# Performance work log

Hardware: AMD Instinct MI355X
Metric: run time of the kernel (lower is better)

## Reference

```python
import jax, jax.numpy as jnp
import numpy as np

B, C, H, W = 4, 64, 256, 256
P = 8            # patch size for rfft2 correlation
THETA = 10000.0  # RoPE base
EPS = 1e-6       # RMSNorm eps


def setup_inputs() -> dict:
    key = jax.random.key(0)
    ks = jax.random.split(key, 4)
    s = 0.05
    return {
        "x": jax.random.normal(ks[0], (B, C, H, W), jnp.float32),
        "w_hidden": jax.random.normal(ks[1], (6 * C, C), jnp.float32) * s,   # 1x1 conv dim->6dim
        "w_dw": jax.random.normal(ks[2], (6 * C, 1, 3, 3), jnp.float32) * s,  # depthwise 3x3
        "w_proj": jax.random.normal(ks[3], (C, 2 * C), jnp.float32) * s,      # 1x1 conv 2dim->dim
        "g_norm": jnp.ones((2 * C,), jnp.float32),
        "g_qnorm": jnp.ones((2 * C,), jnp.float32),
        "g_knorm": jnp.ones((2 * C,), jnp.float32),
    }


def _rms2d(x, w):
    # RMSNorm over channel dim of (B,C,H,W), computed in fp32, learned scale w[C]
    xf = x.astype(jnp.float32)
    var = jnp.mean(xf * xf, axis=1, keepdims=True)
    return w[None, :, None, None] * (xf * jax.lax.rsqrt(var + EPS))


def _rope2d(x):
    # 2D RoPE on (B, 2d, H, W): first d channels get row freqs, last d get col freqs.
    b, c2, h, w = x.shape
    d = c2 // 2
    n = d // 2
    inv = 1.0 / (THETA ** (jnp.arange(0, d, 2, dtype=jnp.float32)[:n] / d))  # (d//2,)
    fh = jnp.repeat(jnp.arange(h, dtype=jnp.float32)[:, None] * inv, 2, axis=-1)  # (h, d)
    fw = jnp.repeat(jnp.arange(w, dtype=jnp.float32)[:, None] * inv, 2, axis=-1)  # (w, d)
    freqs = jnp.concatenate(
        [jnp.broadcast_to(fh[:, None, :], (h, w, d)),
         jnp.broadcast_to(fw[None, :, :], (h, w, d))], axis=-1)  # (h, w, 2d)
    cos = jnp.moveaxis(jnp.cos(freqs), -1, 0)[None]  # (1, 2d, h, w)
    sin = jnp.moveaxis(jnp.sin(freqs), -1, 0)[None]
    xr = x.reshape(b, c2 // 2, 2, h, w)
    rot = jnp.stack([-xr[:, :, 1], xr[:, :, 0]], axis=2).reshape(b, c2, h, w)  # rotate_half
    return x * cos + rot * sin


def reference(x, w_hidden, w_dw, w_proj, g_norm, g_qnorm, g_knorm):
    # FSAS_V5 forward: 1x1 expand -> DW conv -> split q,k,v -> QK RMSNorm -> 2D RoPE
    # -> per-8x8-patch rfft2 correlation -> RMSNorm -> v * corr -> 1x1 project
    hidden = jnp.einsum('oi,bihw->bohw', w_hidden, x)
    hidden = jax.lax.conv_general_dilated(
        hidden, w_dw, window_strides=(1, 1), padding=((1, 1), (1, 1)),
        feature_group_count=w_dw.shape[0],
        dimension_numbers=('NCHW', 'OIHW', 'NCHW'))
    q, k, v = jnp.split(hidden, 3, axis=1)  # each (B, 2C, H, W)
    q = _rope2d(_rms2d(q, g_qnorm))
    k = _rope2d(_rms2d(k, g_knorm))
    bs, c2, hh, ww = q.shape
    h, w = hh // P, ww // P

    def to_patch(t):  # (b,c,H,W) -> (b,c,h,w,P,P)
        return t.reshape(bs, c2, h, P, w, P).transpose(0, 1, 2, 4, 3, 5)

    corr = jnp.fft.irfft2(jnp.fft.rfft2(to_patch(q)) * jnp.fft.rfft2(to_patch(k)), s=(P, P))
    corr = corr.transpose(0, 1, 2, 4, 3, 5).reshape(bs, c2, hh, ww)
    corr = _rms2d(corr, g_norm)
    return jnp.einsum('oi,bihw->bohw', w_proj, v * corr)
```

## Files before the change

### kernel.cpp

```cpp
#include <hip/hip_runtime.h>
#include <math.h>

#define BB 4
#define Cc 64
#define C2 128
#define C6 384
#define HW 65536
#define EPS 1e-6f
#define CST 68
#define OSPLIT 4
#define OGPB 12

__global__ void k_tab(float2* __restrict__ tab) {
    int idx = blockIdx.x * 256 + threadIdx.x;
    if (idx >= 256 * 32) return;
    int r = idx >> 5, m = idx & 31;
    float inv = expf(-((2.0f * (float)m) / 64.0f) * logf(10000.0f));
    float s, c;
    sincosf((float)r * inv, &s, &c);
    tab[idx] = make_float2(c, s);
}

__global__ void k_wt(const float* __restrict__ wp, float* __restrict__ wpt) {
    int t = blockIdx.x * 256 + threadIdx.x;
    if (t >= 64 * 128) return;
    int o = t >> 7, cc = t & 127;
    wpt[cc * 64 + o] = wp[o * 128 + cc];
}

__global__ __launch_bounds__(256, 2) void k_expdw(const float* __restrict__ xb,
                                                  const float* __restrict__ wh,
                                                  const float* __restrict__ wdw,
                                                  float* __restrict__ h2s,
                                                  int r0, int R, int tiles_y) {
    __shared__ float hs[8 * 256];
    int t = threadIdx.x;
    int tx = t & 15, ty = t >> 4;
    int blk = blockIdx.x;
    int txi = blk % 19;
    int rest = blk / 19;
    int tyi = rest % tiles_y;
    int os = rest / tiles_y;
    int r = r0 + tyi * 14 - 1 + ty;
    int c = txi * 14 - 1 + tx;
    int rcl = min(max(r, 0), 255), ccl = min(max(c, 0), 255);
    float xr[64];
    const float* xp = xb + rcl * 256 + ccl;
#pragma unroll
    for (int i = 0; i < 64; i++) xr[i] = xp[(size_t)i * HW];
    bool interior = (ty >= 1 && ty <= 14 && tx >= 1 && tx <= 14 &&
                     r < r0 + R && r < 256 && c < 256);
    size_t SR = (size_t)R * 256;
    for (int ogl = 0; ogl < OGPB; ogl++) {
        int og = os * OGPB + ogl;
#pragma unroll
        for (int oo = 0; oo < 8; oo++) {
            int o = og * 8 + oo;
            const float* wrow = wh + o * 64;
            float a0 = 0.f, a1 = 0.f;
#pragma unroll
            for (int i = 0; i < 64; i += 2) {
                a0 = fmaf(wrow[i], xr[i], a0);
                a1 = fmaf(wrow[i + 1], xr[i + 1], a1);
            }
            hs[oo * 256 + t] = a0 + a1;
        }
        __syncthreads();
        if (interior) {
#pragma unroll
            for (int oo = 0; oo < 8; oo++) {
                int o = og * 8 + oo;
                const float* wk = wdw + o * 9;
                float acc = 0.f;
#pragma unroll
                for (int dr = -1; dr <= 1; dr++) {
                    int rr = r + dr;
                    if (rr < 0 || rr > 255) continue;
#pragma unroll
                    for (int dc = -1; dc <= 1; dc++) {
                        int cc2 = c + dc;
                        if (cc2 < 0 || cc2 > 255) continue;
                        acc = fmaf(wk[(dr + 1) * 3 + dc + 1],
                                   hs[oo * 256 + (ty + dr) * 16 + tx + dc], acc);
                    }
                }
                h2s[(size_t)o * SR + (size_t)(r - r0) * 256 + c] = acc;
            }
        }
        __syncthreads();
    }
}

__global__ __launch_bounds__(256, 2) void k_patch(const float* __restrict__ h2s,
                                                  const float* __restrict__ gq,
                                                  const float* __restrict__ gk,
                                                  const float* __restrict__ gn,
                                                  const float* __restrict__ wpt,
                                                  const float2* __restrict__ tab,
                                                  float* __restrict__ outb,
                                                  int r0, int R) {
    __shared__ float qs[C2 * CST];
    __shared__ float ks[C2 * CST];
    __shared__ float part[256], part2[256];
    __shared__ float sq[64], sk[64], scal[64];
    int t = threadIdx.x;
    int p = blockIdx.x;
    int prs = p >> 5, pc = p & 31;
    size_t SR = (size_t)R * 256;
    size_t sb = (size_t)(prs * 8) * 256 + pc * 8;
    const float* qg = h2s + sb;
    const float* kg = h2s + 128 * SR + sb;
    const float* vg = h2s + 256 * SR + sb;

    for (int it = 0; it < 8; it++) {
        int l4 = it * 256 + t;
        int c = l4 >> 4, r4 = l4 & 15;
        int i = r4 >> 1, jq = r4 & 1;
        *(float4*)&qs[c * CST + i * 8 + jq * 4] = *(const float4*)(qg + (size_t)c * SR + i * 256 + jq * 4);
        *(float4*)&ks[c * CST + i * 8 + jq * 4] = *(const float4*)(kg + (size_t)c * SR + i * 256 + jq * 4);
    }
    __syncthreads();

    {
        int pos = t & 63, grp = t >> 6;
        float s1 = 0.f, s2 = 0.f;
        for (int c = grp * 32; c < grp * 32 + 32; c++) {
            float a = qs[c * CST + pos]; s1 = fmaf(a, a, s1);
            float e = ks[c * CST + pos]; s2 = fmaf(e, e, s2);
        }
        part[grp * 64 + pos] = s1;
        part2[grp * 64 + pos] = s2;
    }
    __syncthreads();
    if (t < 64) {
        sq[t] = rsqrtf((part[t] + part[64 + t] + part[128 + t] + part[192 + t]) * (1.f / 128.f) + EPS);
    } else if (t < 128) {
        int u = t - 64;
        sk[u] = rsqrtf((part2[u] + part2[64 + u] + part2[128 + u] + part2[192 + u]) * (1.f / 128.f) + EPS);
    }
    __syncthreads();

    for (int u = 0; u < 16; u++) {
        int task = u * 256 + t;
        int m = task >> 6, pos = task & 63;
        int i = pos >> 3, j = pos & 7;
        float2 cs = (m < 32) ? tab[(r0 + prs * 8 + i) * 32 + m]
                             : tab[(pc * 8 + j) * 32 + (m - 32)];
        float sqp = sq[pos], skp = sk[pos];
        float q0 = qs[(2 * m) * CST + pos], q1 = qs[(2 * m + 1) * CST + pos];
        float y0 = gq[2 * m] * q0 * sqp, y1 = gq[2 * m + 1] * q1 * sqp;
        qs[(2 * m) * CST + pos] = y0 * cs.x - y1 * cs.y;
        qs[(2 * m + 1) * CST + pos] = y1 * cs.x + y0 * cs.y;
        float k0 = ks[(2 * m) * CST + pos], k1 = ks[(2 * m + 1) * CST + pos];
        float z0 = gk[2 * m] * k0 * skp, z1 = gk[2 * m + 1] * k1 * skp;
        ks[(2 * m) * CST + pos] = z0 * cs.x - z1 * cs.y;
        ks[(2 * m + 1) * CST + pos] = z1 * cs.x + z0 * cs.y;
    }
    __syncthreads();

    float creg[4][8];
#pragma unroll
    for (int g4 = 0; g4 < 4; g4++) {
        int task = g4 * 256 + t;
        int c = task >> 3, m = task & 7;
        float o8[8] = {0, 0, 0, 0, 0, 0, 0, 0};
#pragma unroll
        for (int i = 0; i < 8; i++) {
            const float* qr = &qs[c * CST + i * 8];
            float4 qa = *(const float4*)qr, qb = *(const float4*)(qr + 4);
            float qq[8] = {qa.x, qa.y, qa.z, qa.w, qb.x, qb.y, qb.z, qb.w};
            int kr = (m - i) & 7;
            const float* krp = &ks[c * CST + kr * 8];
            float4 ka = *(const float4*)krp, kb2 = *(const float4*)(krp + 4);
            float kk[8] = {ka.x, ka.y, ka.z, ka.w, kb2.x, kb2.y, kb2.z, kb2.w};
#pragma unroll
            for (int n = 0; n < 8; n++)
#pragma unroll
                for (int j = 0; j < 8; j++)
                    o8[n] = fmaf(qq[j], kk[(n - j) & 7], o8[n]);
        }
#pragma unroll
        for (int n = 0; n < 8; n++) creg[g4][n] = o8[n];
    }
    __syncthreads();

#pragma unroll
    for (int g4 = 0; g4 < 4; g4++) {
        int task = g4 * 256 + t;
        int c = task >> 3, m = task & 7;
        *(float4*)&qs[c * CST + m * 8] =
            make_float4(creg[g4][0], creg[g4][1], creg[g4][2], creg[g4][3]);
        *(float4*)&qs[c * CST + m * 8 + 4] =
            make_float4(creg[g4][4], creg[g4][5], creg[g4][6], creg[g4][7]);
    }
    __syncthreads();

    {
        int pos = t & 63, q4 = t >> 6;
        float ssum = 0.f;
        for (int c = q4 * 32; c < q4 * 32 + 32; c++) {
            float v = qs[c * CST + pos];
            ssum = fmaf(v, v, ssum);
        }
        part[q4 * 64 + pos] = ssum;
    }
    __syncthreads();
    if (t < 64) {
        float s = part[t] + part[64 + t] + part[128 + t] + part[192 + t];
        scal[t] = rsqrtf(s * (1.0f / 128.f) + EPS);
    }
    __syncthreads();

    for (int it = 0; it < 8; it++) {
        int l4 = it * 256 + t;
        int c = l4 >> 4, r4 = l4 & 15;
        int i = r4 >> 1, jq = r4 & 1;
        float4 vv = *(const float4*)(vg + (size_t)c * SR + i * 256 + jq * 4);
        float4 sc4 = *(const float4*)&scal[r4 * 4];
        float g = gn[c];
        float4 cu = *(float4*)&qs[c * CST + r4 * 4];
        cu.x = cu.x * sc4.x * g * vv.x;
        cu.y = cu.y * sc4.y * g * vv.y;
        cu.z = cu.z * sc4.z * g * vv.z;
        cu.w = cu.w * sc4.w * g * vv.w;
        *(float4*)&qs[c * CST + r4 * 4] = cu;
    }
    __syncthreads();

    {
        int o = t & 63, pg = t >> 6;
        float acc[16];
#pragma unroll
        for (int u = 0; u < 16; u++) acc[u] = 0.f;
        for (int c = 0; c < C2; c++) {
            float w = wpt[c * 64 + o];
            const float* tp = &qs[c * CST + pg * 16];
#pragma unroll
            for (int u4 = 0; u4 < 4; u4++) {
                float4 tv = *(const float4*)(tp + u4 * 4);
                acc[u4 * 4 + 0] = fmaf(w, tv.x, acc[u4 * 4 + 0]);
                acc[u4 * 4 + 1] = fmaf(w, tv.y, acc[u4 * 4 + 1]);
                acc[u4 * 4 + 2] = fmaf(w, tv.z, acc[u4 * 4 + 2]);
                acc[u4 * 4 + 3] = fmaf(w, tv.w, acc[u4 * 4 + 3]);
            }
        }
#pragma unroll
        for (int u = 0; u < 16; u++) ks[(pg * 16 + u) * CST + o] = acc[u];
    }
    __syncthreads();

    float* og = outb + (size_t)r0 * 256 + sb;
    for (int it = 0; it < 4; it++) {
        int l4 = it * 256 + t;
        int o = l4 >> 4, r4 = l4 & 15;
        int i = r4 >> 1, jq = r4 & 1;
        int p0 = i * 8 + jq * 4;
        float4 vv = make_float4(ks[(p0 + 0) * CST + o], ks[(p0 + 1) * CST + o],
                                ks[(p0 + 2) * CST + o], ks[(p0 + 3) * CST + o]);
        *(float4*)(og + (size_t)o * HW + i * 256 + jq * 4) = vv;
    }
}

extern "C" void kernel_launch(void* const* d_in, const int* in_sizes, int n_in,
                              void* d_out, int out_size, void* d_ws, size_t ws_size,
                              hipStream_t stream) {
    const float* x   = (const float*)d_in[0];
    const float* wh  = (const float*)d_in[1];
    const float* wdw = (const float*)d_in[2];
    const float* wp  = (const float*)d_in[3];
    const float* gn  = (const float*)d_in[4];
    const float* gq  = (const float*)d_in[5];
    const float* gk  = (const float*)d_in[6];
    float* out = (float*)d_out;

    size_t avail = ws_size / 4;
    if (avail < (size_t)24576 + (size_t)C6 * 8 * 256) return;
    size_t rows_cap = (avail - 24576) / ((size_t)C6 * 256);
    int R = (rows_cap >= 256) ? 256 : (int)(rows_cap & ~(size_t)7);

    float* ws = (float*)d_ws;
    float2* tab = (float2*)ws;
    float* wpt  = ws + 16384;
    float* h2s  = ws + 24576;

    k_tab<<<32, 256, 0, stream>>>(tab);
    k_wt<<<32, 256, 0, stream>>>(wp, wpt);
    for (int b = 0; b < BB; b++) {
        const float* xb = x + (size_t)b * Cc * HW;
        float* outb = out + (size_t)b * Cc * HW;
        for (int r0 = 0; r0 < 256; r0 += R) {
            int Rc = (256 - r0 < R) ? (256 - r0) : R;
            int tiles_y = (Rc + 13) / 14;
            k_expdw<<<19 * tiles_y * OSPLIT, 256, 0, stream>>>(xb, wh, wdw, h2s, r0, Rc, tiles_y);
            k_patch<<<(Rc / 8) * 32, 256, 0, stream>>>(h2s, gq, gk, gn, wpt, tab, outb, r0, Rc);
        }
    }
}
```

Baseline: 1.190 ms.

## Restage expand+depthwise kernel through swizzled shared input tile with double-buffered hidden

The fused 1x1-expand plus depthwise-conv kernel now loads the 64-channel input halo tile into XOR-swizzled shared memory and reads it as float4, instead of holding 64 registers per thread. It also changes the tile from 16x16 to 8x16 threads (6 interior rows) and each block covers 24 output groups instead of 12. The hidden-activation buffer is double-buffered, which drops one barrier per group. The depthwise step computes 8 channels per tap from vectorised shared loads. The goal is lower register pressure and fewer barriers, at the cost of more halo recomputation, since smaller tiles carry a larger overlap fraction.

New measurement: 1.739 ms. 46.1% more time.

```diff
diff --git a/kernel.cpp b/kernel.cpp
--- a/kernel.cpp
+++ b/kernel.cpp
@@ -8,8 +8,6 @@
 #define HW 65536
 #define EPS 1e-6f
 #define CST 68
-#define OSPLIT 4
-#define OGPB 12
 
 __global__ void k_tab(float2* __restrict__ tab) {
     int idx = blockIdx.x * 256 + threadIdx.x;
@@ -28,66 +26,92 @@
     wpt[cc * 64 + o] = wp[o * 128 + cc];
 }
 
-__global__ __launch_bounds__(256, 2) void k_expdw(const float* __restrict__ xb,
-                                                  const float* __restrict__ wh,
-                                                  const float* __restrict__ wdw,
-                                                  float* __restrict__ h2s,
-                                                  int r0, int R, int tiles_y) {
-    __shared__ float hs[8 * 256];
+__global__ __launch_bounds__(128) void k_expdw(const float* __restrict__ xb,
+                                               const float* __restrict__ wh,
+                                               const float* __restrict__ wdw,
+                                               float* __restrict__ h2s,
+                                               int r0, int R, int tiles_y) {
+    __shared__ float xs[128 * 64];
+    __shared__ float hs[2][128 * 8];
     int t = threadIdx.x;
-    int tx = t & 15, ty = t >> 4;
+    int px = t & 15, py = t >> 4;
     int blk = blockIdx.x;
     int txi = blk % 19;
     int rest = blk / 19;
     int tyi = rest % tiles_y;
     int os = rest / tiles_y;
-    int r = r0 + tyi * 14 - 1 + ty;
-    int c = txi * 14 - 1 + tx;
-    int rcl = min(max(r, 0), 255), ccl = min(max(c, 0), 255);
-    float xr[64];
-    const float* xp = xb + rcl * 256 + ccl;
-#pragma unroll
-    for (int i = 0; i < 64; i++) xr[i] = xp[(size_t)i * HW];
-    bool interior = (ty >= 1 && ty <= 14 && tx >= 1 && tx <= 14 &&
-                     r < r0 + R && r < 256 && c < 256);
+    int r = r0 + tyi * 6 - 1 + py;
+    int c = txi * 14 - 1 + px;
+
+    for (int j = 0; j < 16; j++) {
+        int u = j * 128 + t;
+        int p2 = u & 127;
+        int g = u >> 7;
+        int rr = r0 + tyi * 6 - 1 + (p2 >> 4);
+        int cc = txi * 14 - 1 + (p2 & 15);
+        int rcl = min(max(rr, 0), 255), ccl = min(max(cc, 0), 255);
+        const float* gp = xb + (size_t)(g * 4) * HW + rcl * 256 + ccl;
+        float4 v;
+        v.x = gp[0]; v.y = gp[HW]; v.z = gp[2 * HW]; v.w = gp[3 * HW];
+        *(float4*)&xs[p2 * 64 + ((g ^ (p2 & 15)) << 2)] = v;
+    }
+    __syncthreads();
+
+    bool interior = (py >= 1 && py <= 6 && px >= 1 && px <= 14 &&
+                     (r - r0) < R && c <= 255);
     size_t SR = (size_t)R * 256;
-    for (int ogl = 0; ogl < OGPB; ogl++) {
-        int og = os * OGPB + ogl;
-#pragma unroll
-        for (int oo = 0; oo < 8; oo++) {
-            int o = og * 8 + oo;
-            const float* wrow = wh + o * 64;
-            float a0 = 0.f, a1 = 0.f;
-#pragma unroll
-            for (int i = 0; i < 64; i += 2) {
-                a0 = fmaf(wrow[i], xr[i], a0);
-                a1 = fmaf(wrow[i + 1], xr[i + 1], a1);
+    size_t obase = (size_t)(r - r0) * 256 + c;
+
+    for (int ogl = 0; ogl < 24; ogl++) {
+        int og = os * 24 + ogl;
+        float acc[8];
+#pragma unroll
+        for (int oo = 0; oo < 8; oo++) acc[oo] = 0.f;
+#pragma unroll
+        for (int g2 = 0; g2 < 16; g2++) {
+            float4 xv = *(const float4*)&xs[t * 64 + ((g2 ^ (t & 15)) << 2)];
+            const float* wrow = wh + (og * 8) * 64 + g2 * 4;
+#pragma unroll
+            for (int oo = 0; oo < 8; oo++) {
+                acc[oo] = fmaf(wrow[oo * 64 + 0], xv.x, acc[oo]);
+                acc[oo] = fmaf(wrow[oo * 64 + 1], xv.y, acc[oo]);
+                acc[oo] = fmaf(wrow[oo * 64 + 2], xv.z, acc[oo]);
+                acc[oo] = fmaf(wrow[oo * 64 + 3], xv.w, acc[oo]);
             }
-            hs[oo * 256 + t] = a0 + a1;
-        }
+        }
+        float* hb = hs[ogl & 1];
+        *(float4*)&hb[t * 8]     = make_float4(acc[0], acc[1], acc[2], acc[3]);
+        *(float4*)&hb[t * 8 + 4] = make_float4(acc[4], acc[5], acc[6], acc[7]);
         __syncthreads();
         if (interior) {
-#pragma unroll
-            for (int oo = 0; oo < 8; oo++) {
-                int o = og * 8 + oo;
-                const float* wk = wdw + o * 9;
-                float acc = 0.f;
-#pragma unroll
-                for (int dr = -1; dr <= 1; dr++) {
-                    int rr = r + dr;
-                    if (rr < 0 || rr > 255) continue;
-#pragma unroll
-                    for (int dc = -1; dc <= 1; dc++) {
-                        int cc2 = c + dc;
-                        if (cc2 < 0 || cc2 > 255) continue;
-                        acc = fmaf(wk[(dr + 1) * 3 + dc + 1],
-                                   hs[oo * 256 + (ty + dr) * 16 + tx + dc], acc);
-                    }
+            float a[8] = {0, 0, 0, 0, 0, 0, 0, 0};
+            const float* wk = wdw + (og * 8) * 9;
+#pragma unroll
+            for (int dr = -1; dr <= 1; dr++) {
+                int rr = r + dr;
+                bool rok = (rr >= 0 && rr <= 255);
+#pragma unroll
+                for (int dc = -1; dc <= 1; dc++) {
+                    int cc2 = c + dc;
+                    if (!rok || cc2 < 0 || cc2 > 255) continue;
+                    int npos = t + dr * 16 + dc;
+                    float4 h0 = *(const float4*)&hb[npos * 8];
+                    float4 h1 = *(const float4*)&hb[npos * 8 + 4];
+                    int tap = (dr + 1) * 3 + dc + 1;
+                    a[0] = fmaf(wk[0 * 9 + tap], h0.x, a[0]);
+                    a[1] = fmaf(wk[1 * 9 + tap], h0.y, a[1]);
+                    a[2] = fmaf(wk[2 * 9 + tap], h0.z, a[2]);
+                    a[3] = fmaf(wk[3 * 9 + tap], h0.w, a[3]);
+                    a[4] = fmaf(wk[4 * 9 + tap], h1.x, a[4]);
+                    a[5] = fmaf(wk[5 * 9 + tap], h1.y, a[5]);
+                    a[6] = fmaf(wk[6 * 9 + tap], h1.z, a[6]);
+                    a[7] = fmaf(wk[7 * 9 + tap], h1.w, a[7]);
                 }
-                h2s[(size_t)o * SR + (size_t)(r - r0) * 256 + c] = acc;
             }
-        }
-        __syncthreads();
+#pragma unroll
+            for (int oo = 0; oo < 8; oo++)
+                h2s[(size_t)(og * 8 + oo) * SR + obase] = a[oo];
+        }
     }
 }
 
@@ -290,8 +314,8 @@
         float* outb = out + (size_t)b * Cc * HW;
         for (int r0 = 0; r0 < 256; r0 += R) {
             int Rc = (256 - r0 < R) ? (256 - r0) : R;
-            int tiles_y = (Rc + 13) / 14;
-            k_expdw<<<19 * tiles_y * OSPLIT, 256, 0, stream>>>(xb, wh, wdw, h2s, r0, Rc, tiles_y);
+            int tiles_y = (Rc + 5) / 6;
+            k_expdw<<<19 * tiles_y * 2, 128, 0, stream>>>(xb, wh, wdw, h2s, r0, Rc, tiles_y);
             k_patch<<<(Rc / 8) * 32, 256, 0, stream>>>(h2s, gq, gk, gn, wpt, tab, outb, r0, Rc);
         }
     }
```
